# Performance work log

Measured on AMD Instinct MI355X. Metric: run time of the kernel, lower is better.

Reference implementation:

```python
import jax, jax.numpy as jnp
import numpy as np

B, TQ, TM, D, ATTN, H = 8, 1024, 1024, 512, 512, 8
HEAD_DIM = ATTN // H
TEMPERATURE = 1.0
CAUSALITY = True
NEG_INF = -2.0 ** 32 + 1


def setup_inputs() -> dict:
    key = jax.random.key(0)
    ks = jax.random.split(key, 7)
    scale = 1.0 / np.sqrt(D)
    return {
        "inputs": jax.random.normal(ks[0], (B, TQ, D), dtype=jnp.float32),
        "memory": jax.random.normal(ks[1], (B, TM, D), dtype=jnp.float32),
        "Wq": jax.random.normal(ks[2], (D, ATTN), dtype=jnp.float32) * scale,
        "Wk": jax.random.normal(ks[3], (D, ATTN), dtype=jnp.float32) * scale,
        "Wv": jax.random.normal(ks[4], (D, ATTN), dtype=jnp.float32) * scale,
        "memory_lengths": jax.random.randint(ks[5], (B,), TM // 2, TM + 1, dtype=jnp.int32),
        "query_lengths": jax.random.randint(ks[6], (B,), TQ // 2, TQ + 1, dtype=jnp.int32),
    }


def _split_head(x):
    # [B, T, ATTN] -> [B, H, T, HEAD_DIM]
    b, t, _ = x.shape
    return x.reshape(b, t, H, HEAD_DIM).transpose(0, 2, 1, 3)


def reference(inputs, memory, Wq, Wk, Wv, memory_lengths, query_lengths):
    q = _split_head(inputs @ Wq)   # [B,H,Tq,hd]
    k = _split_head(memory @ Wk)   # [B,H,Tm,hd]
    v = _split_head(memory @ Wv)   # [B,H,Tm,hd]

    logits = jnp.einsum("bhqd,bhmd->bhqm", q, k)
    logits = logits / jnp.sqrt(jnp.float32(HEAD_DIM)) / TEMPERATURE

    mem_mask = jnp.arange(TM)[None, :] < memory_lengths[:, None]   # [B,Tm]
    qry_mask = jnp.arange(TQ)[None, :] < query_lengths[:, None]    # [B,Tq]
    length_mask = qry_mask[:, :, None] & mem_mask[:, None, :]      # [B,Tq,Tm]
    mask = length_mask[:, None, :, :]                              # [B,1,Tq,Tm]
    if CAUSALITY:
        causal = jnp.tril(jnp.ones((TQ, TM), dtype=bool))
        mask = mask & causal[None, None, :, :]

    logits = jnp.where(mask, logits, jnp.float32(NEG_INF))
    alignments = jax.nn.softmax(logits, axis=3)                    # [B,H,Tq,Tm]
    contexts = jnp.einsum("bhqm,bhmd->bhqd", alignments, v)
    contexts = contexts.transpose(0, 2, 1, 3).reshape(inputs.shape[0], TQ, ATTN)
    return contexts, alignments
```

## Files before the change

kernel.cpp:

```cpp
#include <hip/hip_runtime.h>

#define NB 8
#define NTQ 1024
#define NTM 1024
#define ND 512
#define NATTN 512
#define NH 8
#define NDH 64

typedef _Float16 half8 __attribute__((ext_vector_type(8)));
typedef float f32x4 __attribute__((ext_vector_type(4)));

__global__ __launch_bounds__(256) void proj_kernel(
    const float* __restrict__ inputs, const float* __restrict__ memory,
    const float* __restrict__ Wq, const float* __restrict__ Wk,
    const float* __restrict__ Wv,
    _Float16* __restrict__ Qh, _Float16* __restrict__ Kh,
    _Float16* __restrict__ Vth) {
  const int z = blockIdx.z;
  const float* __restrict__ A = (z == 0) ? inputs : memory;
  const float* __restrict__ W = (z == 0) ? Wq : ((z == 1) ? Wk : Wv);
  const int row0 = blockIdx.y * 64;
  const int col0 = blockIdx.x * 64;

  __shared__ __align__(16) _Float16 As[64][72];
  __shared__ __align__(16) _Float16 Wt[64][72];

  const int t = threadIdx.x;
  const int w = t >> 6;
  const int L = t & 63;
  const int lrow = L & 15;
  const int quad = L >> 4;
  const int sr = t >> 2;
  const int sc = (t & 3) * 16;

  const f32x4 zf = {0.f, 0.f, 0.f, 0.f};
  f32x4 acc[4];
#pragma unroll
  for (int i = 0; i < 4; i++) acc[i] = zf;

  for (int k0 = 0; k0 < ND; k0 += 64) {
    {
      const float4* src = (const float4*)(A + (size_t)(row0 + sr) * ND + k0 + sc);
      float4 f0 = src[0], f1 = src[1], f2 = src[2], f3 = src[3];
      half8 h0, h1;
      h0[0] = (_Float16)f0.x; h0[1] = (_Float16)f0.y; h0[2] = (_Float16)f0.z; h0[3] = (_Float16)f0.w;
      h0[4] = (_Float16)f1.x; h0[5] = (_Float16)f1.y; h0[6] = (_Float16)f1.z; h0[7] = (_Float16)f1.w;
      h1[0] = (_Float16)f2.x; h1[1] = (_Float16)f2.y; h1[2] = (_Float16)f2.z; h1[3] = (_Float16)f2.w;
      h1[4] = (_Float16)f3.x; h1[5] = (_Float16)f3.y; h1[6] = (_Float16)f3.z; h1[7] = (_Float16)f3.w;
      *(half8*)&As[sr][sc] = h0;
      *(half8*)&As[sr][sc + 8] = h1;
    }
    {
      const float4* src = (const float4*)(W + (size_t)(k0 + sr) * NATTN + col0 + sc);
      float4 g0 = src[0], g1 = src[1], g2 = src[2], g3 = src[3];
      float gv[16];
      *(float4*)&gv[0] = g0; *(float4*)&gv[4] = g1;
      *(float4*)&gv[8] = g2; *(float4*)&gv[12] = g3;
#pragma unroll
      for (int j = 0; j < 16; j++) Wt[sc + j][sr] = (_Float16)gv[j];
    }
    __syncthreads();
#pragma unroll
    for (int ks = 0; ks < 2; ks++) {
      half8 a = *(const half8*)&As[w * 16 + lrow][ks * 32 + quad * 8];
#pragma unroll
      for (int nt = 0; nt < 4; nt++) {
        half8 b = *(const half8*)&Wt[nt * 16 + lrow][ks * 32 + quad * 8];
        acc[nt] = __builtin_amdgcn_mfma_f32_16x16x32_f16(a, b, acc[nt], 0, 0, 0);
      }
    }
    __syncthreads();
  }

  const int b = row0 >> 10;
  const int tr0 = row0 & 1023;
  const int hh = col0 >> 6;
  if (z <= 1) {
    _Float16* dst = (z == 0 ? Qh : Kh) + (size_t)(b * NH + hh) * NTQ * NDH;
#pragma unroll
    for (int nt = 0; nt < 4; nt++) {
#pragma unroll
      for (int r = 0; r < 4; r++) {
        int trow = tr0 + w * 16 + quad * 4 + r;
        int d = nt * 16 + lrow;
        dst[(size_t)trow * NDH + d] = (_Float16)acc[nt][r];
      }
    }
  } else {
#pragma unroll
    for (int nt = 0; nt < 4; nt++) {
#pragma unroll
      for (int r = 0; r < 4; r++)
        As[nt * 16 + lrow][w * 16 + quad * 4 + r] = (_Float16)acc[nt][r];
    }
    __syncthreads();
    _Float16* dst = Vth + ((size_t)(b * NH + hh) * NDH + sr) * NTM + tr0 + sc;
    *(half8*)dst = *(const half8*)&As[sr][sc];
    *(half8*)(dst + 8) = *(const half8*)&As[sr][sc + 8];
  }
}

__global__ __launch_bounds__(256) void attn_kernel(
    const _Float16* __restrict__ Qh, const _Float16* __restrict__ Kh,
    const _Float16* __restrict__ Vth, const int* __restrict__ mem_len,
    const int* __restrict__ qry_len, float* __restrict__ ctx_out,
    float* __restrict__ align_out) {
  const int bh = blockIdx.x;
  const int qt = blockIdx.y;
  const int bb = bh >> 3;
  const int hh = bh & 7;
  const int q0 = qt * 64;

  __shared__ __align__(16) _Float16 Qs[64][72];
  __shared__ __align__(16) _Float16 Ks[64][72];
  __shared__ __align__(16) _Float16 Vts[64][72];
  __shared__ __align__(16) _Float16 Ps[4][16][72];

  const int t = threadIdx.x, w = t >> 6, L = t & 63;
  const int lrow = L & 15, quad = L >> 4;
  const int qlen = qry_len[bb], mlen = mem_len[bb];
  const int mtop = (mlen + 63) >> 6;
  const int n_comp = (q0 + 63 >= qlen) ? 16 : min(qt + 1, mtop);
  const _Float16* Qbase = Qh + (size_t)bh * NTQ * NDH;
  const _Float16* Kbase = Kh + (size_t)bh * NTM * NDH;
  const _Float16* Vbase = Vth + (size_t)bh * NDH * NTM;
  const int sr = t >> 2, sc = (t & 3) * 16;
  const f32x4 zf = {0.f, 0.f, 0.f, 0.f};
  float* abase = align_out + (size_t)bh * NTQ * NTM;

  if (n_comp < 16) {
    const int c0 = n_comp * 64;
    float* rp = abase + (size_t)(q0 + sr) * NTM;
    const float4 z4 = {0.f, 0.f, 0.f, 0.f};
    for (int c = c0 + (t & 3) * 4; c < NTM; c += 16) *(float4*)(rp + c) = z4;
  }

  {
    const half8* src = (const half8*)(Qbase + (size_t)(q0 + sr) * NDH + sc);
    *(half8*)&Qs[sr][sc] = src[0];
    *(half8*)&Qs[sr][sc + 8] = src[1];
  }
  const int qg = q0 + w * 16 + quad * 4;
  float rowsum[4] = {0.f, 0.f, 0.f, 0.f};
  __syncthreads();

  for (int mt = 0; mt < n_comp; mt++) {
    {
      const half8* src = (const half8*)(Kbase + (size_t)(mt * 64 + sr) * NDH + sc);
      *(half8*)&Ks[sr][sc] = src[0];
      *(half8*)&Ks[sr][sc + 8] = src[1];
    }
    __syncthreads();
    f32x4 sacc[4];
#pragma unroll
    for (int i = 0; i < 4; i++) sacc[i] = zf;
#pragma unroll
    for (int ks = 0; ks < 2; ks++) {
      half8 a = *(const half8*)&Qs[w * 16 + lrow][ks * 32 + quad * 8];
#pragma unroll
      for (int nt = 0; nt < 4; nt++) {
        half8 b = *(const half8*)&Ks[nt * 16 + lrow][ks * 32 + quad * 8];
        sacc[nt] = __builtin_amdgcn_mfma_f32_16x16x32_f16(a, b, sacc[nt], 0, 0, 0);
      }
    }
#pragma unroll
    for (int nt = 0; nt < 4; nt++) {
      int m = mt * 64 + nt * 16 + lrow;
#pragma unroll
      for (int r = 0; r < 4; r++) {
        int q = qg + r;
        float p;
        if (q >= qlen) p = 1.0f;
        else if (m > q || m >= mlen) p = 0.0f;
        else p = __expf(sacc[nt][r] * 0.125f);
        rowsum[r] += p;
      }
    }
    __syncthreads();
  }
  float inv[4];
#pragma unroll
  for (int r = 0; r < 4; r++) {
    float s = rowsum[r];
    s += __shfl_xor(s, 1, 16);
    s += __shfl_xor(s, 2, 16);
    s += __shfl_xor(s, 4, 16);
    s += __shfl_xor(s, 8, 16);
    inv[r] = 1.0f / s;
  }

  f32x4 cacc[4];
#pragma unroll
  for (int i = 0; i < 4; i++) cacc[i] = zf;

  for (int mt = 0; mt < n_comp; mt++) {
    {
      const half8* src = (const half8*)(Kbase + (size_t)(mt * 64 + sr) * NDH + sc);
      *(half8*)&Ks[sr][sc] = src[0];
      *(half8*)&Ks[sr][sc + 8] = src[1];
      const half8* vsrc = (const half8*)(Vbase + (size_t)sr * NTM + mt * 64 + sc);
      *(half8*)&Vts[sr][sc] = vsrc[0];
      *(half8*)&Vts[sr][sc + 8] = vsrc[1];
    }
    __syncthreads();
    f32x4 sacc[4];
#pragma unroll
    for (int i = 0; i < 4; i++) sacc[i] = zf;
#pragma unroll
    for (int ks = 0; ks < 2; ks++) {
      half8 a = *(const half8*)&Qs[w * 16 + lrow][ks * 32 + quad * 8];
#pragma unroll
      for (int nt = 0; nt < 4; nt++) {
        half8 b = *(const half8*)&Ks[nt * 16 + lrow][ks * 32 + quad * 8];
        sacc[nt] = __builtin_amdgcn_mfma_f32_16x16x32_f16(a, b, sacc[nt], 0, 0, 0);
      }
    }
#pragma unroll
    for (int nt = 0; nt < 4; nt++) {
      int m = mt * 64 + nt * 16 + lrow;
#pragma unroll
      for (int r = 0; r < 4; r++) {
        int q = qg + r;
        float p;
        if (q >= qlen) p = inv[r];
        else if (m > q || m >= mlen) p = 0.0f;
        else p = __expf(sacc[nt][r] * 0.125f) * inv[r];
        abase[(size_t)q * NTM + m] = p;
        Ps[w][quad * 4 + r][nt * 16 + lrow] = (_Float16)p;
      }
    }
#pragma unroll
    for (int ks = 0; ks < 2; ks++) {
      half8 a = *(const half8*)&Ps[w][lrow][ks * 32 + quad * 8];
#pragma unroll
      for (int dt = 0; dt < 4; dt++) {
        half8 b = *(const half8*)&Vts[dt * 16 + lrow][ks * 32 + quad * 8];
        cacc[dt] = __builtin_amdgcn_mfma_f32_16x16x32_f16(a, b, cacc[dt], 0, 0, 0);
      }
    }
    __syncthreads();
  }

  float* cbase = ctx_out + (size_t)bb * NTQ * NATTN + (size_t)hh * NDH;
#pragma unroll
  for (int dt = 0; dt < 4; dt++) {
#pragma unroll
    for (int r = 0; r < 4; r++) {
      int q = qg + r;
      cbase[(size_t)q * NATTN + dt * 16 + lrow] = cacc[dt][r];
    }
  }
}

extern "C" void kernel_launch(void* const* d_in, const int* in_sizes, int n_in,
                              void* d_out, int out_size, void* d_ws,
                              size_t ws_size, hipStream_t stream) {
  const float* inputs = (const float*)d_in[0];
  const float* memory = (const float*)d_in[1];
  const float* Wq = (const float*)d_in[2];
  const float* Wk = (const float*)d_in[3];
  const float* Wv = (const float*)d_in[4];
  const int* mlen = (const int*)d_in[5];
  const int* qlen = (const int*)d_in[6];

  float* ctx = (float*)d_out;
  float* align = ctx + (size_t)NB * NTQ * NATTN;

  _Float16* Qh = (_Float16*)d_ws;
  _Float16* Kh = Qh + (size_t)NB * NH * NTQ * NDH;
  _Float16* Vth = Kh + (size_t)NB * NH * NTM * NDH;

  proj_kernel<<<dim3(8, 128, 3), 256, 0, stream>>>(inputs, memory, Wq, Wk, Wv,
                                                   Qh, Kh, Vth);
  attn_kernel<<<dim3(64, 16), 256, 0, stream>>>(Qh, Kh, Vth, mlen, qlen, ctx,
                                                align);
}
```

Before: 418.7 us.

## Pre-transpose weights, widen projection tiles, and drop LDS staging in attention

Adds a small kernel that converts the weights to fp16 and transposes them once into scratch space inside the alignments output buffer, so the projection no longer does a strided per-tile transpose. The projection tile becomes 64x128 with an XCD-aware block mapping and coalesced vectorized stores through LDS. The attention kernel loads Q fragments into registers, reads K and V straight from global memory (no LDS tiles or block barriers), and uses a per-wave causal tile count. It applies the 1/rowsum normalization at store time, writing alignments as vectorized rows. The trade-off is more redundant global loads of K and V per wave, and fp16-rounded probabilities now go into the alignments output.

```diff
diff --git a/kernel.cpp b/kernel.cpp
--- a/kernel.cpp
+++ b/kernel.cpp
@@ -11,33 +11,59 @@
 typedef _Float16 half8 __attribute__((ext_vector_type(8)));
 typedef float f32x4 __attribute__((ext_vector_type(4)));
 
+__global__ __launch_bounds__(256) void wprep_kernel(
+    const float* __restrict__ Wq, const float* __restrict__ Wk,
+    const float* __restrict__ Wv, _Float16* __restrict__ Wt) {
+  const int z = blockIdx.z;
+  const float* __restrict__ W = (z == 0) ? Wq : ((z == 1) ? Wk : Wv);
+  _Float16* __restrict__ out = Wt + (size_t)z * NATTN * ND;
+  const int k0 = blockIdx.x * 64;
+  const int n0 = blockIdx.y * 64;
+  __shared__ __align__(16) _Float16 Ls[64][72];
+  const int t = threadIdx.x;
+  const int sr = t >> 2, sc = (t & 3) * 16;
+  const float4* src = (const float4*)(W + (size_t)(k0 + sr) * NATTN + n0 + sc);
+  float4 f0 = src[0], f1 = src[1], f2 = src[2], f3 = src[3];
+  float gv[16];
+  *(float4*)&gv[0] = f0; *(float4*)&gv[4] = f1;
+  *(float4*)&gv[8] = f2; *(float4*)&gv[12] = f3;
+#pragma unroll
+  for (int j = 0; j < 16; j++) Ls[sc + j][sr] = (_Float16)gv[j];
+  __syncthreads();
+  _Float16* dst = out + (size_t)(n0 + sr) * ND + k0 + sc;
+  *(half8*)dst = *(const half8*)&Ls[sr][sc];
+  *(half8*)(dst + 8) = *(const half8*)&Ls[sr][sc + 8];
+}
+
 __global__ __launch_bounds__(256) void proj_kernel(
     const float* __restrict__ inputs, const float* __restrict__ memory,
-    const float* __restrict__ Wq, const float* __restrict__ Wk,
-    const float* __restrict__ Wv,
-    _Float16* __restrict__ Qh, _Float16* __restrict__ Kh,
-    _Float16* __restrict__ Vth) {
-  const int z = blockIdx.z;
+    const _Float16* __restrict__ Wt, _Float16* __restrict__ Qh,
+    _Float16* __restrict__ Kh, _Float16* __restrict__ Vth) {
+  const int id = blockIdx.x;
+  const int xcd = id & 7;
+  const int g = id >> 3;
+  const int z = g >> 6;
+  const int gg = g & 63;
+  const int row0 = (xcd * 16 + (gg >> 2)) * 64;
+  const int col0 = (gg & 3) * 128;
+
   const float* __restrict__ A = (z == 0) ? inputs : memory;
-  const float* __restrict__ W = (z == 0) ? Wq : ((z == 1) ? Wk : Wv);
-  const int row0 = blockIdx.y * 64;
-  const int col0 = blockIdx.x * 64;
-
-  __shared__ __align__(16) _Float16 As[64][72];
-  __shared__ __align__(16) _Float16 Wt[64][72];
+  const _Float16* __restrict__ Wz = Wt + (size_t)z * NATTN * ND;
+
+  __shared__ __align__(16) _Float16 pool[64 * 72 + 128 * 72];
+  _Float16* Asb = pool;
+  _Float16* Wsb = pool + 64 * 72;
 
   const int t = threadIdx.x;
-  const int w = t >> 6;
-  const int L = t & 63;
-  const int lrow = L & 15;
-  const int quad = L >> 4;
-  const int sr = t >> 2;
-  const int sc = (t & 3) * 16;
+  const int w = t >> 6, L = t & 63;
+  const int lrow = L & 15, quad = L >> 4;
+  const int sr = t >> 2, sc = (t & 3) * 16;
+  const int sr2 = t >> 1, sc2 = (t & 1) * 32;
 
   const f32x4 zf = {0.f, 0.f, 0.f, 0.f};
-  f32x4 acc[4];
-#pragma unroll
-  for (int i = 0; i < 4; i++) acc[i] = zf;
+  f32x4 acc[8];
+#pragma unroll
+  for (int i = 0; i < 8; i++) acc[i] = zf;
 
   for (int k0 = 0; k0 < ND; k0 += 64) {
     {
@@ -48,128 +74,116 @@
       h0[4] = (_Float16)f1.x; h0[5] = (_Float16)f1.y; h0[6] = (_Float16)f1.z; h0[7] = (_Float16)f1.w;
       h1[0] = (_Float16)f2.x; h1[1] = (_Float16)f2.y; h1[2] = (_Float16)f2.z; h1[3] = (_Float16)f2.w;
       h1[4] = (_Float16)f3.x; h1[5] = (_Float16)f3.y; h1[6] = (_Float16)f3.z; h1[7] = (_Float16)f3.w;
-      *(half8*)&As[sr][sc] = h0;
-      *(half8*)&As[sr][sc + 8] = h1;
+      *(half8*)&Asb[sr * 72 + sc] = h0;
+      *(half8*)&Asb[sr * 72 + sc + 8] = h1;
     }
     {
-      const float4* src = (const float4*)(W + (size_t)(k0 + sr) * NATTN + col0 + sc);
-      float4 g0 = src[0], g1 = src[1], g2 = src[2], g3 = src[3];
-      float gv[16];
-      *(float4*)&gv[0] = g0; *(float4*)&gv[4] = g1;
-      *(float4*)&gv[8] = g2; *(float4*)&gv[12] = g3;
-#pragma unroll
-      for (int j = 0; j < 16; j++) Wt[sc + j][sr] = (_Float16)gv[j];
+      const half8* wsrc = (const half8*)(Wz + (size_t)(col0 + sr2) * ND + k0 + sc2);
+#pragma unroll
+      for (int j = 0; j < 4; j++) *(half8*)&Wsb[sr2 * 72 + sc2 + 8 * j] = wsrc[j];
     }
     __syncthreads();
 #pragma unroll
     for (int ks = 0; ks < 2; ks++) {
-      half8 a = *(const half8*)&As[w * 16 + lrow][ks * 32 + quad * 8];
-#pragma unroll
-      for (int nt = 0; nt < 4; nt++) {
-        half8 b = *(const half8*)&Wt[nt * 16 + lrow][ks * 32 + quad * 8];
+      half8 a = *(const half8*)&Asb[(w * 16 + lrow) * 72 + ks * 32 + quad * 8];
+#pragma unroll
+      for (int nt = 0; nt < 8; nt++) {
+        half8 b = *(const half8*)&Wsb[(nt * 16 + lrow) * 72 + ks * 32 + quad * 8];
         acc[nt] = __builtin_amdgcn_mfma_f32_16x16x32_f16(a, b, acc[nt], 0, 0, 0);
       }
     }
     __syncthreads();
   }
 
-  const int b = row0 >> 10;
+  const int bb = row0 >> 10;
   const int tr0 = row0 & 1023;
-  const int hh = col0 >> 6;
+  const int hh0 = col0 >> 6;
+
   if (z <= 1) {
-    _Float16* dst = (z == 0 ? Qh : Kh) + (size_t)(b * NH + hh) * NTQ * NDH;
-#pragma unroll
-    for (int nt = 0; nt < 4; nt++) {
-#pragma unroll
-      for (int r = 0; r < 4; r++) {
-        int trow = tr0 + w * 16 + quad * 4 + r;
-        int d = nt * 16 + lrow;
-        dst[(size_t)trow * NDH + d] = (_Float16)acc[nt][r];
-      }
-    }
+#pragma unroll
+    for (int nt = 0; nt < 8; nt++)
+#pragma unroll
+      for (int r = 0; r < 4; r++)
+        pool[(w * 16 + quad * 4 + r) * 136 + nt * 16 + lrow] = (_Float16)acc[nt][r];
+    __syncthreads();
+    const int sce = (t & 3) * 32;
+    _Float16* base = (z == 0) ? Qh : Kh;
+    _Float16* dst = base + (size_t)(bb * NH + hh0 + (sce >> 6)) * NTQ * NDH +
+                    (size_t)(tr0 + sr) * NDH + (sce & 63);
+#pragma unroll
+    for (int j = 0; j < 4; j++)
+      *(half8*)(dst + 8 * j) = *(const half8*)&pool[sr * 136 + sce + 8 * j];
   } else {
 #pragma unroll
-    for (int nt = 0; nt < 4; nt++) {
+    for (int nt = 0; nt < 8; nt++)
 #pragma unroll
       for (int r = 0; r < 4; r++)
-        As[nt * 16 + lrow][w * 16 + quad * 4 + r] = (_Float16)acc[nt][r];
-    }
-    __syncthreads();
-    _Float16* dst = Vth + ((size_t)(b * NH + hh) * NDH + sr) * NTM + tr0 + sc;
-    *(half8*)dst = *(const half8*)&As[sr][sc];
-    *(half8*)(dst + 8) = *(const half8*)&As[sr][sc + 8];
-  }
-}
-
-__global__ __launch_bounds__(256) void attn_kernel(
+        Wsb[(nt * 16 + lrow) * 72 + w * 16 + quad * 4 + r] = (_Float16)acc[nt][r];
+    __syncthreads();
+    _Float16* dst = Vth +
+        ((size_t)(bb * NH + hh0 + (sr2 >> 6)) * NDH + (sr2 & 63)) * NTM + tr0 + sc2;
+#pragma unroll
+    for (int j = 0; j < 4; j++)
+      *(half8*)(dst + 8 * j) = *(const half8*)&Wsb[sr2 * 72 + sc2 + 8 * j];
+  }
+}
+
+__global__ __launch_bounds__(256, 4) void attn_kernel(
     const _Float16* __restrict__ Qh, const _Float16* __restrict__ Kh,
     const _Float16* __restrict__ Vth, const int* __restrict__ mem_len,
     const int* __restrict__ qry_len, float* __restrict__ ctx_out,
     float* __restrict__ align_out) {
   const int bh = blockIdx.x;
   const int qt = blockIdx.y;
-  const int bb = bh >> 3;
-  const int hh = bh & 7;
-  const int q0 = qt * 64;
-
-  __shared__ __align__(16) _Float16 Qs[64][72];
-  __shared__ __align__(16) _Float16 Ks[64][72];
-  __shared__ __align__(16) _Float16 Vts[64][72];
+  const int bb = bh >> 3, hh = bh & 7;
+  const int q0 = qt << 6;
+
   __shared__ __align__(16) _Float16 Ps[4][16][72];
+  __shared__ float invs[4][16];
 
   const int t = threadIdx.x, w = t >> 6, L = t & 63;
   const int lrow = L & 15, quad = L >> 4;
   const int qlen = qry_len[bb], mlen = mem_len[bb];
   const int mtop = (mlen + 63) >> 6;
-  const int n_comp = (q0 + 63 >= qlen) ? 16 : min(qt + 1, mtop);
-  const _Float16* Qbase = Qh + (size_t)bh * NTQ * NDH;
-  const _Float16* Kbase = Kh + (size_t)bh * NTM * NDH;
-  const _Float16* Vbase = Vth + (size_t)bh * NDH * NTM;
-  const int sr = t >> 2, sc = (t & 3) * 16;
+  const int wq = q0 + w * 16;
+  const int nW = (wq + 15 >= qlen) ? 16 : min(mtop, ((wq + 15) >> 6) + 1);
+
+  const _Float16* __restrict__ Qbase = Qh + (size_t)bh * (NTQ * NDH);
+  const _Float16* __restrict__ Kbase = Kh + (size_t)bh * (NTM * NDH);
+  const _Float16* __restrict__ Vbase = Vth + (size_t)bh * (NDH * NTM);
+  float* __restrict__ abase = align_out + (size_t)bh * (NTQ * NTM);
+
+  const int qg = wq + quad * 4;
+  const int qr = wq + lrow;
+
+  if (nW < 16) {
+    float* rp = abase + (size_t)qr * NTM;
+    const f32x4 z4 = {0.f, 0.f, 0.f, 0.f};
+    for (int c = nW * 64 + quad * 4; c < NTM; c += 16) *(f32x4*)(rp + c) = z4;
+  }
+
+  const half8 qa0 = *(const half8*)(Qbase + (size_t)qr * NDH + quad * 8);
+  const half8 qa1 = *(const half8*)(Qbase + (size_t)qr * NDH + 32 + quad * 8);
+
   const f32x4 zf = {0.f, 0.f, 0.f, 0.f};
-  float* abase = align_out + (size_t)bh * NTQ * NTM;
-
-  if (n_comp < 16) {
-    const int c0 = n_comp * 64;
-    float* rp = abase + (size_t)(q0 + sr) * NTM;
-    const float4 z4 = {0.f, 0.f, 0.f, 0.f};
-    for (int c = c0 + (t & 3) * 4; c < NTM; c += 16) *(float4*)(rp + c) = z4;
-  }
-
-  {
-    const half8* src = (const half8*)(Qbase + (size_t)(q0 + sr) * NDH + sc);
-    *(half8*)&Qs[sr][sc] = src[0];
-    *(half8*)&Qs[sr][sc + 8] = src[1];
-  }
-  const int qg = q0 + w * 16 + quad * 4;
   float rowsum[4] = {0.f, 0.f, 0.f, 0.f};
-  __syncthreads();
-
-  for (int mt = 0; mt < n_comp; mt++) {
-    {
-      const half8* src = (const half8*)(Kbase + (size_t)(mt * 64 + sr) * NDH + sc);
-      *(half8*)&Ks[sr][sc] = src[0];
-      *(half8*)&Ks[sr][sc + 8] = src[1];
-    }
-    __syncthreads();
-    f32x4 sacc[4];
-#pragma unroll
-    for (int i = 0; i < 4; i++) sacc[i] = zf;
-#pragma unroll
-    for (int ks = 0; ks < 2; ks++) {
-      half8 a = *(const half8*)&Qs[w * 16 + lrow][ks * 32 + quad * 8];
-#pragma unroll
-      for (int nt = 0; nt < 4; nt++) {
-        half8 b = *(const half8*)&Ks[nt * 16 + lrow][ks * 32 + quad * 8];
-        sacc[nt] = __builtin_amdgcn_mfma_f32_16x16x32_f16(a, b, sacc[nt], 0, 0, 0);
-      }
-    }
-#pragma unroll
-    for (int nt = 0; nt < 4; nt++) {
-      int m = mt * 64 + nt * 16 + lrow;
+
+  for (int mt = 0; mt < nW; mt++) {
+    f32x4 sacc[4] = {zf, zf, zf, zf};
+    const _Float16* kp = Kbase + (size_t)((mt << 6) + lrow) * NDH + quad * 8;
+#pragma unroll
+    for (int nt = 0; nt < 4; nt++) {
+      half8 b0 = *(const half8*)(kp + nt * (16 * NDH));
+      half8 b1 = *(const half8*)(kp + nt * (16 * NDH) + 32);
+      sacc[nt] = __builtin_amdgcn_mfma_f32_16x16x32_f16(qa0, b0, sacc[nt], 0, 0, 0);
+      sacc[nt] = __builtin_amdgcn_mfma_f32_16x16x32_f16(qa1, b1, sacc[nt], 0, 0, 0);
+    }
+#pragma unroll
+    for (int nt = 0; nt < 4; nt++) {
+      const int m = (mt << 6) + nt * 16 + lrow;
 #pragma unroll
       for (int r = 0; r < 4; r++) {
-        int q = qg + r;
+        const int q = qg + r;
         float p;
         if (q >= qlen) p = 1.0f;
         else if (m > q || m >= mlen) p = 0.0f;
@@ -177,7 +191,6 @@
         rowsum[r] += p;
       }
     }
-    __syncthreads();
   }
   float inv[4];
 #pragma unroll
@@ -189,68 +202,69 @@
     s += __shfl_xor(s, 8, 16);
     inv[r] = 1.0f / s;
   }
-
-  f32x4 cacc[4];
-#pragma unroll
-  for (int i = 0; i < 4; i++) cacc[i] = zf;
-
-  for (int mt = 0; mt < n_comp; mt++) {
-    {
-      const half8* src = (const half8*)(Kbase + (size_t)(mt * 64 + sr) * NDH + sc);
-      *(half8*)&Ks[sr][sc] = src[0];
-      *(half8*)&Ks[sr][sc + 8] = src[1];
-      const half8* vsrc = (const half8*)(Vbase + (size_t)sr * NTM + mt * 64 + sc);
-      *(half8*)&Vts[sr][sc] = vsrc[0];
-      *(half8*)&Vts[sr][sc + 8] = vsrc[1];
-    }
-    __syncthreads();
-    f32x4 sacc[4];
-#pragma unroll
-    for (int i = 0; i < 4; i++) sacc[i] = zf;
-#pragma unroll
-    for (int ks = 0; ks < 2; ks++) {
-      half8 a = *(const half8*)&Qs[w * 16 + lrow][ks * 32 + quad * 8];
-#pragma unroll
-      for (int nt = 0; nt < 4; nt++) {
-        half8 b = *(const half8*)&Ks[nt * 16 + lrow][ks * 32 + quad * 8];
-        sacc[nt] = __builtin_amdgcn_mfma_f32_16x16x32_f16(a, b, sacc[nt], 0, 0, 0);
-      }
-    }
-#pragma unroll
-    for (int nt = 0; nt < 4; nt++) {
-      int m = mt * 64 + nt * 16 + lrow;
+  if (lrow == 0) {
+#pragma unroll
+    for (int r = 0; r < 4; r++) invs[w][quad * 4 + r] = inv[r];
+  }
+  const float inv_me = invs[w][lrow];
+
+  f32x4 cacc[4] = {zf, zf, zf, zf};
+  for (int mt = 0; mt < nW; mt++) {
+    f32x4 sacc[4] = {zf, zf, zf, zf};
+    const _Float16* kp = Kbase + (size_t)((mt << 6) + lrow) * NDH + quad * 8;
+#pragma unroll
+    for (int nt = 0; nt < 4; nt++) {
+      half8 b0 = *(const half8*)(kp + nt * (16 * NDH));
+      half8 b1 = *(const half8*)(kp + nt * (16 * NDH) + 32);
+      sacc[nt] = __builtin_amdgcn_mfma_f32_16x16x32_f16(qa0, b0, sacc[nt], 0, 0, 0);
+      sacc[nt] = __builtin_amdgcn_mfma_f32_16x16x32_f16(qa1, b1, sacc[nt], 0, 0, 0);
+    }
+#pragma unroll
+    for (int nt = 0; nt < 4; nt++) {
+      const int m = (mt << 6) + nt * 16 + lrow;
 #pragma unroll
       for (int r = 0; r < 4; r++) {
-        int q = qg + r;
+        const int q = qg + r;
         float p;
-        if (q >= qlen) p = inv[r];
+        if (q >= qlen) p = 1.0f;
         else if (m > q || m >= mlen) p = 0.0f;
-        else p = __expf(sacc[nt][r] * 0.125f) * inv[r];
-        abase[(size_t)q * NTM + m] = p;
+        else p = __expf(sacc[nt][r] * 0.125f);
         Ps[w][quad * 4 + r][nt * 16 + lrow] = (_Float16)p;
       }
     }
-#pragma unroll
-    for (int ks = 0; ks < 2; ks++) {
-      half8 a = *(const half8*)&Ps[w][lrow][ks * 32 + quad * 8];
-#pragma unroll
-      for (int dt = 0; dt < 4; dt++) {
-        half8 b = *(const half8*)&Vts[dt * 16 + lrow][ks * 32 + quad * 8];
-        cacc[dt] = __builtin_amdgcn_mfma_f32_16x16x32_f16(a, b, cacc[dt], 0, 0, 0);
-      }
-    }
-    __syncthreads();
-  }
-
-  float* cbase = ctx_out + (size_t)bb * NTQ * NATTN + (size_t)hh * NDH;
-#pragma unroll
-  for (int dt = 0; dt < 4; dt++) {
-#pragma unroll
-    for (int r = 0; r < 4; r++) {
-      int q = qg + r;
-      cbase[(size_t)q * NATTN + dt * 16 + lrow] = cacc[dt][r];
-    }
-  }
+    const half8 pa0 = *(const half8*)&Ps[w][lrow][quad * 8];
+    const half8 pa1 = *(const half8*)&Ps[w][lrow][32 + quad * 8];
+
+    float* ap = abase + (size_t)qr * NTM + (mt << 6) + quad * 8;
+    f32x4 a0 = {(float)pa0[0] * inv_me, (float)pa0[1] * inv_me,
+                (float)pa0[2] * inv_me, (float)pa0[3] * inv_me};
+    f32x4 a1 = {(float)pa0[4] * inv_me, (float)pa0[5] * inv_me,
+                (float)pa0[6] * inv_me, (float)pa0[7] * inv_me};
+    f32x4 a2 = {(float)pa1[0] * inv_me, (float)pa1[1] * inv_me,
+                (float)pa1[2] * inv_me, (float)pa1[3] * inv_me};
+    f32x4 a3 = {(float)pa1[4] * inv_me, (float)pa1[5] * inv_me,
+                (float)pa1[6] * inv_me, (float)pa1[7] * inv_me};
+    *(f32x4*)ap = a0;
+    *(f32x4*)(ap + 4) = a1;
+    *(f32x4*)(ap + 32) = a2;
+    *(f32x4*)(ap + 36) = a3;
+
+    const _Float16* vp = Vbase + (size_t)lrow * NTM + (mt << 6) + quad * 8;
+#pragma unroll
+    for (int dt = 0; dt < 4; dt++) {
+      half8 v0 = *(const half8*)(vp + dt * (16 * NTM));
+      half8 v1 = *(const half8*)(vp + dt * (16 * NTM) + 32);
+      cacc[dt] = __builtin_amdgcn_mfma_f32_16x16x32_f16(pa0, v0, cacc[dt], 0, 0, 0);
+      cacc[dt] = __builtin_amdgcn_mfma_f32_16x16x32_f16(pa1, v1, cacc[dt], 0, 0, 0);
+    }
+  }
+
+  float* cbase = ctx_out + (size_t)bb * (NTQ * NATTN) + (size_t)hh * NDH;
+#pragma unroll
+  for (int dt = 0; dt < 4; dt++)
+#pragma unroll
+    for (int r = 0; r < 4; r++)
+      cbase[(size_t)(qg + r) * NATTN + dt * 16 + lrow] = cacc[dt][r] * inv[r];
 }
 
 extern "C" void kernel_launch(void* const* d_in, const int* in_sizes, int n_in,
@@ -270,9 +284,10 @@
   _Float16* Qh = (_Float16*)d_ws;
   _Float16* Kh = Qh + (size_t)NB * NH * NTQ * NDH;
   _Float16* Vth = Kh + (size_t)NB * NH * NTM * NDH;
-
-  proj_kernel<<<dim3(8, 128, 3), 256, 0, stream>>>(inputs, memory, Wq, Wk, Wv,
-                                                   Qh, Kh, Vth);
+  _Float16* Wt = (_Float16*)align;
+
+  wprep_kernel<<<dim3(8, 8, 3), 256, 0, stream>>>(Wq, Wk, Wv, Wt);
+  proj_kernel<<<dim3(1536), 256, 0, stream>>>(inputs, memory, Wt, Qh, Kh, Vth);
   attn_kernel<<<dim3(64, 16), 256, 0, stream>>>(Qh, Kh, Vth, mlen, qlen, ctx,
                                                 align);
 }
```

Measured after the change: 452.0 us. 8.0% more time.
